# Kernel optimization log

Measured on AMD Instinct MI355X. Metric: run time of the kernel, lower is better.

The kernel has to match this reference:

```python
import jax, jax.numpy as jnp
import numpy as np

L, B, E, H = 512, 4, 512, 8
D = E // H  # head_dim = 64


def setup_inputs() -> dict:
    key = jax.random.key(0)
    ks = jax.random.split(key, 7)
    query = jax.random.normal(ks[0], (L, B, E), dtype=jnp.float32)
    relation_k = jax.random.normal(ks[1], (B, L, L, D), dtype=jnp.float32)
    relation_v = jax.random.normal(ks[2], (B, L, L, D), dtype=jnp.float32)
    # xavier-uniform-ish scale for the fused QKV projection
    lim = float(np.sqrt(6.0 / (3 * E + E)))
    in_proj_weight = jax.random.uniform(ks[3], (3 * E, E), jnp.float32, -lim, lim)
    in_proj_bias = jnp.zeros((3 * E,), jnp.float32)
    lim_o = float(np.sqrt(1.0 / E))
    out_proj_weight = jax.random.uniform(ks[4], (E, E), jnp.float32, -lim_o, lim_o)
    out_proj_bias = jnp.zeros((E,), jnp.float32)
    return {
        "query": query,
        "relation_k": relation_k,
        "relation_v": relation_v,
        "in_proj_weight": in_proj_weight,
        "in_proj_bias": in_proj_bias,
        "out_proj_weight": out_proj_weight,
        "out_proj_bias": out_proj_bias,
    }


def reference(query, relation_k, relation_v, in_proj_weight, in_proj_bias,
              out_proj_weight, out_proj_bias):
    # query == key == value (qkv_same path), shape (L, B, E)
    scaling = float(D) ** -0.5
    qkv = query @ in_proj_weight.T + in_proj_bias          # (L, B, 3E)
    q, k, v = jnp.split(qkv, 3, axis=-1)                   # each (L, B, E)
    q = q * scaling

    def to_bhld(t):  # (L, B, E) -> (B, H, L, D)
        return t.reshape(L, B, H, D).transpose(1, 2, 0, 3)

    q, k, v = to_bhld(q), to_bhld(k), to_bhld(v)

    # content scores
    scores = jnp.einsum('bhid,bhjd->bhij', q, k)           # (B, H, L, L)

    # relation_k term: torch does a flat .view of (B*H, L, L, D) -> (B*H*L, D, L)
    # which is a row-major REINTERPRETATION (not a transpose). Replicate via reshape:
    rk = relation_k.reshape(B, L, D, L)                    # per-(b,i) block (L*D,) -> (D, L)
    scores = scores + jnp.einsum('bhid,bidj->bhij', q, rk)

    w = jax.nn.softmax(scores, axis=-1)
    w = jnp.where(jnp.isnan(w), jnp.zeros_like(w), w)      # NaN guard as in original

    out = jnp.einsum('bhij,bhjd->bhid', w, v)              # (B, H, L, D)
    # relation_v term: (B*H*L, 1, L) @ (B*H*L, L, D) -> per-query weighted relation values
    out = out + jnp.einsum('bhij,bijd->bhid', w, relation_v)

    out = out.transpose(2, 0, 1, 3).reshape(L, B, E)       # (B,H,L,D) -> (L,B,E)
    return out @ out_proj_weight.T + out_proj_bias
```

## Files before the change

kernel.cpp:

```cpp
#include <hip/hip_runtime.h>
#include <hip/hip_fp16.h>
#include <stdint.h>


typedef short short8 __attribute__((ext_vector_type(8)));
typedef float f32x4 __attribute__((ext_vector_type(4)));
typedef unsigned short u16x4 __attribute__((ext_vector_type(4)));

static __device__ __forceinline__ uint16_t f2bf(float f) {
  uint32_t u = __float_as_uint(f);
  uint32_t r = (u + 0x7FFFu + ((u >> 16) & 1u)) >> 16;
  return (uint16_t)r;
}
static __device__ __forceinline__ float bf2f(uint16_t h) {
  return __uint_as_float(((uint32_t)h) << 16);
}
static __device__ __forceinline__ short8 ld8(const uint16_t* p) {
  return *(const short8*)p;
}
#define MFMA(a, b, c) __builtin_amdgcn_mfma_f32_16x16x32_bf16((a), (b), (c), 0, 0, 0)

__global__ __launch_bounds__(256) void k_conv_all(
    const float* __restrict__ in_w, const float* __restrict__ query,
    const float* __restrict__ out_w, uint16_t* __restrict__ w_hi,
    uint16_t* __restrict__ w_lo, uint16_t* __restrict__ a_hi,
    uint16_t* __restrict__ a_lo, uint16_t* __restrict__ wo_bf) {
  int e = (blockIdx.x * 256 + threadIdx.x) * 4;
  if (e < 786432) {
    f32x4 v = *(const f32x4*)(in_w + e);
    u16x4 hi, lo;
#pragma unroll
    for (int k = 0; k < 4; ++k) {
      hi[k] = f2bf(v[k]);
      lo[k] = f2bf(v[k] - bf2f(hi[k]));
    }
    *(u16x4*)(w_hi + e) = hi;
    *(u16x4*)(w_lo + e) = lo;
  } else if (e < 786432 + 1048576) {
    int o = e - 786432;
    f32x4 v = *(const f32x4*)(query + o);
    u16x4 hi, lo;
#pragma unroll
    for (int k = 0; k < 4; ++k) {
      hi[k] = f2bf(v[k]);
      lo[k] = f2bf(v[k] - bf2f(hi[k]));
    }
    *(u16x4*)(a_hi + o) = hi;
    *(u16x4*)(a_lo + o) = lo;
  } else {
    int o = e - 1835008;
    f32x4 v = *(const f32x4*)(out_w + o);
    u16x4 hi;
#pragma unroll
    for (int k = 0; k < 4; ++k) hi[k] = f2bf(v[k]);
    *(u16x4*)(wo_bf + o) = hi;
  }
}

__global__ __launch_bounds__(256) void k_inproj(
    const uint16_t* __restrict__ a_hi, const uint16_t* __restrict__ a_lo,
    const uint16_t* __restrict__ w_hi, const uint16_t* __restrict__ w_lo,
    const float* __restrict__ bias, float* __restrict__ q_s,
    uint16_t* __restrict__ q_bf, uint16_t* __restrict__ k_bf,
    uint16_t* __restrict__ v_bf) {
  const int wave = threadIdx.x >> 6, lane = threadIdx.x & 63;
  const int wr = wave >> 1, wc = wave & 1;
  const int rif = lane & 15, kg = lane >> 4;
  const int rbase = blockIdx.x * 64 + wr * 32;
  const int cbase = blockIdx.y * 64 + wc * 32;
  f32x4 acc[2][2] = {};
  for (int ks = 0; ks < 512; ks += 32) {
    int kofs = ks + kg * 8;
    short8 aH[2], aL[2], bH[2], bL[2];
#pragma unroll
    for (int m = 0; m < 2; ++m) {
      size_t idx = (size_t)(rbase + m * 16 + rif) * 512 + kofs;
      aH[m] = ld8(a_hi + idx);
      aL[m] = ld8(a_lo + idx);
    }
#pragma unroll
    for (int n = 0; n < 2; ++n) {
      size_t idx = (size_t)(cbase + n * 16 + rif) * 512 + kofs;
      bH[n] = ld8(w_hi + idx);
      bL[n] = ld8(w_lo + idx);
    }
#pragma unroll
    for (int m = 0; m < 2; ++m)
#pragma unroll
      for (int n = 0; n < 2; ++n) {
        acc[m][n] = MFMA(aH[m], bH[n], acc[m][n]);
        acc[m][n] = MFMA(aH[m], bL[n], acc[m][n]);
        acc[m][n] = MFMA(aL[m], bH[n], acc[m][n]);
      }
  }
#pragma unroll
  for (int m = 0; m < 2; ++m)
#pragma unroll
    for (int n = 0; n < 2; ++n)
#pragma unroll
      for (int r = 0; r < 4; ++r) {
        int row = rbase + m * 16 + kg * 4 + r;
        int col = cbase + n * 16 + rif;
        float val = acc[m][n][r] + bias[col];
        int l = row >> 2, b = row & 3;
        int sel = col >> 9, h = (col >> 6) & 7, d = col & 63;
        size_t oidx = ((size_t)(b * 8 + h) * 512 + l) * 64 + d;
        if (sel == 0) {
          val *= 0.125f;
          q_s[oidx] = val;
          q_bf[oidx] = f2bf(val);
        } else if (sel == 1) {
          k_bf[oidx] = f2bf(val);
        } else {
          v_bf[oidx] = f2bf(val);
        }
      }
}

__global__ __launch_bounds__(256) void k_scores(const uint16_t* __restrict__ q_bf,
                                                const uint16_t* __restrict__ k_bf,
                                                __half* __restrict__ scores) {
  const int bh = blockIdx.x;
  const uint16_t* qb = q_bf + (size_t)bh * 512 * 64;
  const uint16_t* kb = k_bf + (size_t)bh * 512 * 64;
  const int wave = threadIdx.x >> 6, lane = threadIdx.x & 63;
  const int wr = wave >> 1, wc = wave & 1;
  const int rif = lane & 15, kg = lane >> 4;
  const int ibase = blockIdx.y * 64 + wr * 32;
  const int jbase = blockIdx.z * 64 + wc * 32;
  f32x4 acc[2][2] = {};
#pragma unroll
  for (int ks = 0; ks < 64; ks += 32) {
    int kofs = ks + kg * 8;
    short8 A[2], Bb[2];
#pragma unroll
    for (int m = 0; m < 2; ++m) A[m] = ld8(qb + (size_t)(ibase + m * 16 + rif) * 64 + kofs);
#pragma unroll
    for (int n = 0; n < 2; ++n) Bb[n] = ld8(kb + (size_t)(jbase + n * 16 + rif) * 64 + kofs);
#pragma unroll
    for (int m = 0; m < 2; ++m)
#pragma unroll
      for (int n = 0; n < 2; ++n) acc[m][n] = MFMA(A[m], Bb[n], acc[m][n]);
  }
  __half* sc = scores + (size_t)bh * 512 * 512;
#pragma unroll
  for (int m = 0; m < 2; ++m)
#pragma unroll
    for (int n = 0; n < 2; ++n)
#pragma unroll
      for (int r = 0; r < 4; ++r)
        sc[(size_t)(ibase + m * 16 + kg * 4 + r) * 512 + (jbase + n * 16 + rif)] =
            __float2half(acc[m][n][r]);
}

__global__ __launch_bounds__(256) void k_mega2(
    const float* __restrict__ relation_k, const float* __restrict__ relation_v,
    const float* __restrict__ q_s, const __half* __restrict__ scores,
    uint16_t* __restrict__ wprob, uint16_t* __restrict__ rv_bf) {
  __shared__ float qh[512];
  __shared__ float shr[4608];
  const int b = blockIdx.x >> 9, i = blockIdx.x & 511;
  const int t = threadIdx.x;
  const int wave = t >> 6, lane = t & 63;
  for (int e = t; e < 512; e += 256) {
    int h = e >> 6, d = e & 63;
    qh[d * 8 + h] = q_s[(((size_t)b * 8 + h) * 512 + i) * 64 + d];
  }
  __syncthreads();
  const int H = wave & 1, Dh = wave >> 1;
  const int j0 = H * 256 + lane * 4;
  f32x4 acc[8];
#pragma unroll
  for (int h = 0; h < 8; ++h) acc[h] = f32x4{0.f, 0.f, 0.f, 0.f};
  {
    const float* rkp =
        relation_k + ((size_t)b * 512 + i) * 32768 + (size_t)Dh * 32 * 512 + j0;
    const float* qp = qh + Dh * 32 * 8;
#pragma unroll 2
    for (int dd = 0; dd < 32; ++dd) {
      f32x4 kv = *(const f32x4*)(rkp + (size_t)dd * 512);
      f32x4 qA = *(const f32x4*)(qp + dd * 8);
      f32x4 qB = *(const f32x4*)(qp + dd * 8 + 4);
#pragma unroll
      for (int h = 0; h < 4; ++h) {
        acc[h] += qA[h] * kv;
        acc[4 + h] += qB[h] * kv;
      }
    }
  }
  if (Dh == 1) {
#pragma unroll
    for (int h = 0; h < 8; ++h)
      *(f32x4*)&shr[(H * 64 + lane) * 33 + h * 4] = acc[h];
  }
  __syncthreads();
  if (Dh == 0) {
#pragma unroll
    for (int h = 0; h < 8; ++h)
      acc[h] += *(const f32x4*)&shr[(H * 64 + lane) * 33 + h * 4];
  }
  __syncthreads();
  if (Dh == 0) {
#pragma unroll
    for (int h = 0; h < 8; ++h) *(f32x4*)&shr[h * 512 + j0] = acc[h];
  }
  __syncthreads();
  float ex[2][8], rsum[2];
#pragma unroll
  for (int hh = 0; hh < 2; ++hh) {
    int h = wave * 2 + hh;
    const __half* srow = scores + (((size_t)b * 8 + h) * 512 + i) * 512;
    float s[8], m = -1e30f;
#pragma unroll
    for (int jj = 0; jj < 8; ++jj) {
      int j = jj * 64 + lane;
      s[jj] = __half2float(srow[j]) + shr[h * 512 + j];
      m = fmaxf(m, s[jj]);
    }
    for (int o = 32; o > 0; o >>= 1) m = fmaxf(m, __shfl_xor(m, o));
    float sum = 0.f;
#pragma unroll
    for (int jj = 0; jj < 8; ++jj) {
      ex[hh][jj] = __expf(s[jj] - m);
      sum += ex[hh][jj];
    }
    for (int o = 32; o > 0; o >>= 1) sum += __shfl_xor(sum, o);
    rsum[hh] = 1.f / sum;
  }
#pragma unroll
  for (int hh = 0; hh < 2; ++hh) {
    int h = wave * 2 + hh;
    uint16_t* wrow = wprob + (((size_t)b * 8 + h) * 512 + i) * 512;
#pragma unroll
    for (int jj = 0; jj < 8; ++jj) wrow[jj * 64 + lane] = f2bf(ex[hh][jj] * rsum[hh]);
  }
  __syncthreads();
#pragma unroll
  for (int hh = 0; hh < 2; ++hh) {
    int h = wave * 2 + hh;
#pragma unroll
    for (int jj = 0; jj < 8; ++jj) {
      int j = jj * 64 + lane;
      shr[j * 9 + h] = ex[hh][jj] * rsum[hh];
    }
  }
  __syncthreads();
  f32x4 racc[8];
#pragma unroll
  for (int h = 0; h < 8; ++h) racc[h] = f32x4{0.f, 0.f, 0.f, 0.f};
  {
    const int jsub = lane >> 4, d4 = (lane & 15) * 4;
    const float* rvb = relation_v + ((size_t)b * 512 + i) * 32768;
#pragma unroll 2
    for (int s = 0; s < 32; ++s) {
      int j = s * 16 + wave * 4 + jsub;
      f32x4 rvv = *(const f32x4*)(rvb + (size_t)j * 64 + d4);
      f32x4 w0 = *(const f32x4*)&shr[j * 9];
      f32x4 w1 = *(const f32x4*)&shr[j * 9 + 4];
#pragma unroll
      for (int h = 0; h < 4; ++h) {
        racc[h] += w0[h] * rvv;
        racc[4 + h] += w1[h] * rvv;
      }
    }
  }
#pragma unroll
  for (int h = 0; h < 8; ++h)
#pragma unroll
    for (int c = 0; c < 4; ++c) {
      racc[h][c] += __shfl_xor(racc[h][c], 16);
      racc[h][c] += __shfl_xor(racc[h][c], 32);
    }
  __syncthreads();
  if (lane < 16) {
#pragma unroll
    for (int h = 0; h < 8; ++h)
      *(f32x4*)&shr[(wave * 8 + h) * 64 + (lane & 15) * 4] = racc[h];
  }
  __syncthreads();
  for (int e = t; e < 512; e += 256) {
    int h = e >> 6, d = e & 63;
    float s = shr[(0 * 8 + h) * 64 + d] + shr[(1 * 8 + h) * 64 + d] +
              shr[(2 * 8 + h) * 64 + d] + shr[(3 * 8 + h) * 64 + d];
    rv_bf[((size_t)i * 4 + b) * 512 + h * 64 + d] = f2bf(s);
  }
}

__global__ __launch_bounds__(256) void k_pv(const uint16_t* __restrict__ w_bf,
                                            const uint16_t* __restrict__ v_bf,
                                            uint16_t* __restrict__ pv_bf) {
  const int bh = blockIdx.x;
  const int b = bh >> 3, h = bh & 7;
  const uint16_t* wb = w_bf + (size_t)bh * 512 * 512;
  const uint16_t* vb = v_bf + (size_t)bh * 512 * 64;
  const int wave = threadIdx.x >> 6, lane = threadIdx.x & 63;
  const int wr = wave >> 1, wc = wave & 1;
  const int rif = lane & 15, kg = lane >> 4;
  const int ibase = blockIdx.y * 64 + wr * 32;
  const int dbase = wc * 32;
  f32x4 acc[2][2] = {};
  for (int ks = 0; ks < 512; ks += 32) {
    int kofs = ks + kg * 8;
    short8 A[2], Bb[2];
#pragma unroll
    for (int m = 0; m < 2; ++m) A[m] = ld8(wb + (size_t)(ibase + m * 16 + rif) * 512 + kofs);
#pragma unroll
    for (int n = 0; n < 2; ++n) {
      uint16_t tb[8];
#pragma unroll
      for (int e = 0; e < 8; ++e) tb[e] = vb[(size_t)(kofs + e) * 64 + dbase + n * 16 + rif];
      Bb[n] = *(const short8*)tb;
    }
#pragma unroll
    for (int m = 0; m < 2; ++m)
#pragma unroll
      for (int n = 0; n < 2; ++n) acc[m][n] = MFMA(A[m], Bb[n], acc[m][n]);
  }
#pragma unroll
  for (int m = 0; m < 2; ++m)
#pragma unroll
    for (int n = 0; n < 2; ++n)
#pragma unroll
      for (int r = 0; r < 4; ++r) {
        int i = ibase + m * 16 + kg * 4 + r;
        int d = dbase + n * 16 + rif;
        pv_bf[((size_t)i * 4 + b) * 512 + h * 64 + d] = f2bf(acc[m][n][r]);
      }
}

__global__ __launch_bounds__(256) void k_outproj(const uint16_t* __restrict__ rv_a,
                                                 const uint16_t* __restrict__ pv_a,
                                                 const uint16_t* __restrict__ wo_bf,
                                                 const float* __restrict__ bias,
                                                 float* __restrict__ out) {
  const int wave = threadIdx.x >> 6, lane = threadIdx.x & 63;
  const int wr = wave >> 1, wc = wave & 1;
  const int rif = lane & 15, kg = lane >> 4;
  const int rbase = blockIdx.x * 64 + wr * 32;
  const int cbase = blockIdx.y * 64 + wc * 32;
  f32x4 acc[2][2] = {};
  for (int ks = 0; ks < 512; ks += 32) {
    int kofs = ks + kg * 8;
    short8 A[2], Bb[2];
#pragma unroll
    for (int m = 0; m < 2; ++m) {
      size_t idx = (size_t)(rbase + m * 16 + rif) * 512 + kofs;
      short8 p = ld8(pv_a + idx);
      short8 rr = ld8(rv_a + idx);
      uint16_t tb[8];
#pragma unroll
      for (int e = 0; e < 8; ++e)
        tb[e] = f2bf(bf2f((uint16_t)p[e]) + bf2f((uint16_t)rr[e]));
      A[m] = *(const short8*)tb;
    }
#pragma unroll
    for (int n = 0; n < 2; ++n) Bb[n] = ld8(wo_bf + (size_t)(cbase + n * 16 + rif) * 512 + kofs);
#pragma unroll
    for (int m = 0; m < 2; ++m)
#pragma unroll
      for (int n = 0; n < 2; ++n) acc[m][n] = MFMA(A[m], Bb[n], acc[m][n]);
  }
#pragma unroll
  for (int m = 0; m < 2; ++m)
#pragma unroll
    for (int n = 0; n < 2; ++n)
#pragma unroll
      for (int r = 0; r < 4; ++r) {
        int row = rbase + m * 16 + kg * 4 + r;
        int col = cbase + n * 16 + rif;
        out[(size_t)row * 512 + col] = acc[m][n][r] + bias[col];
      }
}

extern "C" void kernel_launch(void* const* d_in, const int* in_sizes, int n_in,
                              void* d_out, int out_size, void* d_ws, size_t ws_size,
                              hipStream_t stream) {
  const float* query = (const float*)d_in[0];
  const float* relation_k = (const float*)d_in[1];
  const float* relation_v = (const float*)d_in[2];
  const float* in_w = (const float*)d_in[3];
  const float* in_b = (const float*)d_in[4];
  const float* out_w = (const float*)d_in[5];
  const float* out_b = (const float*)d_in[6];
  float* out = (float*)d_out;
  char* ws = (char*)d_ws;

  uint16_t* a_hi  = (uint16_t*)(ws + 0);
  uint16_t* a_lo  = (uint16_t*)(ws + 2097152);
  uint16_t* w_hi  = (uint16_t*)(ws + 4194304);
  uint16_t* w_lo  = (uint16_t*)(ws + 5767168);
  uint16_t* wo_bf = (uint16_t*)(ws + 7340032);
  float*    q_s   = (float*)   (ws + 7864320);
  uint16_t* q_bf  = (uint16_t*)(ws + 12058624);
  uint16_t* k_bf  = (uint16_t*)(ws + 14155776);
  uint16_t* v_bf  = (uint16_t*)(ws + 16252928);
  uint16_t* rv_bf = (uint16_t*)(ws + 18350080);
  uint16_t* pv_bf = (uint16_t*)(ws + 20447232);
  uint16_t* wprob = (uint16_t*)(ws + 22544384);
  __half*   sc_h  = (__half*)  (ws + 39321600);

  k_conv_all<<<dim3(2048), 256, 0, stream>>>(in_w, query, out_w, w_hi, w_lo, a_hi, a_lo, wo_bf);
  k_inproj<<<dim3(32, 24), 256, 0, stream>>>(a_hi, a_lo, w_hi, w_lo, in_b, q_s, q_bf, k_bf, v_bf);
  k_scores<<<dim3(32, 8, 8), 256, 0, stream>>>(q_bf, k_bf, sc_h);
  k_mega2<<<dim3(2048), 256, 0, stream>>>(relation_k, relation_v, q_s, sc_h, wprob, rv_bf);
  k_pv<<<dim3(32, 8), 256, 0, stream>>>(wprob, v_bf, pv_bf);
  k_outproj<<<dim3(32, 8), 256, 0, stream>>>(rv_bf, pv_bf, wo_bf, out_b, out);
}
```

Baseline: 211.8 us.

## Split relation_v accumulation into separate kernel and batch relation loads

Splits the fused relation_k/softmax/relation_v kernel into two kernels. The first computes the relation_k scores and softmax and writes bf16 probabilities. The second reloads those probabilities, transposes them into shared memory and accumulates against relation_v. Both relation streams are now loaded in batches of eight vector loads, with nontemporal hints on relation_k, to raise memory-level parallelism and cut register pressure in each kernel. The cost is an extra launch, a re-read of the probabilities, and relation_v accumulation using bf16-rounded weights instead of fp32.

```diff
diff --git a/kernel.cpp b/kernel.cpp
--- a/kernel.cpp
+++ b/kernel.cpp
@@ -153,10 +153,9 @@
             __float2half(acc[m][n][r]);
 }
 
-__global__ __launch_bounds__(256) void k_mega2(
-    const float* __restrict__ relation_k, const float* __restrict__ relation_v,
-    const float* __restrict__ q_s, const __half* __restrict__ scores,
-    uint16_t* __restrict__ wprob, uint16_t* __restrict__ rv_bf) {
+__global__ __launch_bounds__(256) void k_rksm2(
+    const float* __restrict__ relation_k, const float* __restrict__ q_s,
+    const __half* __restrict__ scores, uint16_t* __restrict__ wprob) {
   __shared__ float qh[512];
   __shared__ float shr[4608];
   const int b = blockIdx.x >> 9, i = blockIdx.x & 511;
@@ -176,15 +175,20 @@
     const float* rkp =
         relation_k + ((size_t)b * 512 + i) * 32768 + (size_t)Dh * 32 * 512 + j0;
     const float* qp = qh + Dh * 32 * 8;
-#pragma unroll 2
-    for (int dd = 0; dd < 32; ++dd) {
-      f32x4 kv = *(const f32x4*)(rkp + (size_t)dd * 512);
-      f32x4 qA = *(const f32x4*)(qp + dd * 8);
-      f32x4 qB = *(const f32x4*)(qp + dd * 8 + 4);
-#pragma unroll
-      for (int h = 0; h < 4; ++h) {
-        acc[h] += qA[h] * kv;
-        acc[4 + h] += qB[h] * kv;
+    for (int dd = 0; dd < 32; dd += 8) {
+      f32x4 kv[8];
+#pragma unroll
+      for (int u = 0; u < 8; ++u)
+        kv[u] = __builtin_nontemporal_load((const f32x4*)(rkp + (size_t)(dd + u) * 512));
+#pragma unroll
+      for (int u = 0; u < 8; ++u) {
+        f32x4 qA = *(const f32x4*)(qp + (dd + u) * 8);
+        f32x4 qB = *(const f32x4*)(qp + (dd + u) * 8 + 4);
+#pragma unroll
+        for (int h = 0; h < 4; ++h) {
+          acc[h] += qA[h] * kv[u];
+          acc[4 + h] += qB[h] * kv[u];
+        }
       }
     }
   }
@@ -205,7 +209,6 @@
     for (int h = 0; h < 8; ++h) *(f32x4*)&shr[h * 512 + j0] = acc[h];
   }
   __syncthreads();
-  float ex[2][8], rsum[2];
 #pragma unroll
   for (int hh = 0; hh < 2; ++hh) {
     int h = wave * 2 + hh;
@@ -218,71 +221,17 @@
       m = fmaxf(m, s[jj]);
     }
     for (int o = 32; o > 0; o >>= 1) m = fmaxf(m, __shfl_xor(m, o));
-    float sum = 0.f;
+    float ex[8], sum = 0.f;
 #pragma unroll
     for (int jj = 0; jj < 8; ++jj) {
-      ex[hh][jj] = __expf(s[jj] - m);
-      sum += ex[hh][jj];
+      ex[jj] = __expf(s[jj] - m);
+      sum += ex[jj];
     }
     for (int o = 32; o > 0; o >>= 1) sum += __shfl_xor(sum, o);
-    rsum[hh] = 1.f / sum;
-  }
-#pragma unroll
-  for (int hh = 0; hh < 2; ++hh) {
-    int h = wave * 2 + hh;
+    float r = 1.f / sum;
     uint16_t* wrow = wprob + (((size_t)b * 8 + h) * 512 + i) * 512;
 #pragma unroll
-    for (int jj = 0; jj < 8; ++jj) wrow[jj * 64 + lane] = f2bf(ex[hh][jj] * rsum[hh]);
-  }
-  __syncthreads();
-#pragma unroll
-  for (int hh = 0; hh < 2; ++hh) {
-    int h = wave * 2 + hh;
-#pragma unroll
-    for (int jj = 0; jj < 8; ++jj) {
-      int j = jj * 64 + lane;
-      shr[j * 9 + h] = ex[hh][jj] * rsum[hh];
-    }
-  }
-  __syncthreads();
-  f32x4 racc[8];
-#pragma unroll
-  for (int h = 0; h < 8; ++h) racc[h] = f32x4{0.f, 0.f, 0.f, 0.f};
-  {
-    const int jsub = lane >> 4, d4 = (lane & 15) * 4;
-    const float* rvb = relation_v + ((size_t)b * 512 + i) * 32768;
-#pragma unroll 2
-    for (int s = 0; s < 32; ++s) {
-      int j = s * 16 + wave * 4 + jsub;
-      f32x4 rvv = *(const f32x4*)(rvb + (size_t)j * 64 + d4);
-      f32x4 w0 = *(const f32x4*)&shr[j * 9];
-      f32x4 w1 = *(const f32x4*)&shr[j * 9 + 4];
-#pragma unroll
-      for (int h = 0; h < 4; ++h) {
-        racc[h] += w0[h] * rvv;
-        racc[4 + h] += w1[h] * rvv;
-      }
-    }
-  }
-#pragma unroll
-  for (int h = 0; h < 8; ++h)
-#pragma unroll
-    for (int c = 0; c < 4; ++c) {
-      racc[h][c] += __shfl_xor(racc[h][c], 16);
-      racc[h][c] += __shfl_xor(racc[h][c], 32);
-    }
-  __syncthreads();
-  if (lane < 16) {
-#pragma unroll
-    for (int h = 0; h < 8; ++h)
-      *(f32x4*)&shr[(wave * 8 + h) * 64 + (lane & 15) * 4] = racc[h];
-  }
-  __syncthreads();
-  for (int e = t; e < 512; e += 256) {
-    int h = e >> 6, d = e & 63;
-    float s = shr[(0 * 8 + h) * 64 + d] + shr[(1 * 8 + h) * 64 + d] +
-              shr[(2 * 8 + h) * 64 + d] + shr[(3 * 8 + h) * 64 + d];
-    rv_bf[((size_t)i * 4 + b) * 512 + h * 64 + d] = f2bf(s);
+    for (int jj = 0; jj < 8; ++jj) wrow[jj * 64 + lane] = f2bf(ex[jj] * r);
   }
 }
 
@@ -328,6 +277,70 @@
       }
 }
 
+__global__ __launch_bounds__(256) void k_rv2(const float* __restrict__ relation_v,
+                                             const uint16_t* __restrict__ wprob,
+                                             uint16_t* __restrict__ rv_bf) {
+  __shared__ float wT[4608];
+  const int b = blockIdx.x >> 9, i = blockIdx.x & 511;
+  const int t = threadIdx.x;
+  const int wave = t >> 6, lane = t & 63;
+  for (int jj = t; jj < 512; jj += 256) {
+    uint16_t tmp[8];
+#pragma unroll
+    for (int h = 0; h < 8; ++h)
+      tmp[h] = wprob[(((size_t)b * 8 + h) * 512 + i) * 512 + jj];
+#pragma unroll
+    for (int h = 0; h < 8; ++h) wT[jj * 9 + h] = bf2f(tmp[h]);
+  }
+  __syncthreads();
+  f32x4 racc[8];
+#pragma unroll
+  for (int h = 0; h < 8; ++h) racc[h] = f32x4{0.f, 0.f, 0.f, 0.f};
+  {
+    const int jsub = lane >> 4, d4 = (lane & 15) * 4;
+    const float* rvb = relation_v + ((size_t)b * 512 + i) * 32768;
+    for (int s8 = 0; s8 < 32; s8 += 8) {
+      f32x4 rvv[8];
+      int js[8];
+#pragma unroll
+      for (int u = 0; u < 8; ++u) {
+        js[u] = (s8 + u) * 16 + wave * 4 + jsub;
+        rvv[u] = *(const f32x4*)(rvb + (size_t)js[u] * 64 + d4);
+      }
+#pragma unroll
+      for (int u = 0; u < 8; ++u) {
+        f32x4 w0 = *(const f32x4*)&wT[js[u] * 9];
+        f32x4 w1 = *(const f32x4*)&wT[js[u] * 9 + 4];
+#pragma unroll
+        for (int h = 0; h < 4; ++h) {
+          racc[h] += w0[h] * rvv[u];
+          racc[4 + h] += w1[h] * rvv[u];
+        }
+      }
+    }
+  }
+#pragma unroll
+  for (int h = 0; h < 8; ++h)
+#pragma unroll
+    for (int c = 0; c < 4; ++c) {
+      racc[h][c] += __shfl_xor(racc[h][c], 16);
+      racc[h][c] += __shfl_xor(racc[h][c], 32);
+    }
+  __syncthreads();
+  if (lane < 16) {
+#pragma unroll
+    for (int h = 0; h < 8; ++h)
+      *(f32x4*)&wT[(wave * 8 + h) * 64 + (lane & 15) * 4] = racc[h];
+  }
+  __syncthreads();
+  for (int e = t; e < 512; e += 256) {
+    int h = e >> 6, d = e & 63;
+    float s = wT[(0 * 8 + h) * 64 + d] + wT[(1 * 8 + h) * 64 + d] +
+              wT[(2 * 8 + h) * 64 + d] + wT[(3 * 8 + h) * 64 + d];
+    rv_bf[((size_t)i * 4 + b) * 512 + h * 64 + d] = f2bf(s);
+  }
+}
+
 __global__ __launch_bounds__(256) void k_outproj(const uint16_t* __restrict__ rv_a,
                                                  const uint16_t* __restrict__ pv_a,
                                                  const uint16_t* __restrict__ wo_bf,
@@ -402,7 +415,8 @@
   k_conv_all<<<dim3(2048), 256, 0, stream>>>(in_w, query, out_w, w_hi, w_lo, a_hi, a_lo, wo_bf);
   k_inproj<<<dim3(32, 24), 256, 0, stream>>>(a_hi, a_lo, w_hi, w_lo, in_b, q_s, q_bf, k_bf, v_bf);
   k_scores<<<dim3(32, 8, 8), 256, 0, stream>>>(q_bf, k_bf, sc_h);
-  k_mega2<<<dim3(2048), 256, 0, stream>>>(relation_k, relation_v, q_s, sc_h, wprob, rv_bf);
+  k_rksm2<<<dim3(2048), 256, 0, stream>>>(relation_k, q_s, sc_h, wprob);
   k_pv<<<dim3(32, 8), 256, 0, stream>>>(wprob, v_bf, pv_bf);
+  k_rv2<<<dim3(2048), 256, 0, stream>>>(relation_v, wprob, rv_bf);
   k_outproj<<<dim3(32, 8), 256, 0, stream>>>(rv_bf, pv_bf, wo_bf, out_b, out);
 }
```

Measured after the change: 198.0 us. 6.5% less time.
